# Optimization experiments

Hardware: AMD Instinct MI355X
Metric: run time of the kernel (lower is better)

Reference implementation:

```python
import jax, jax.numpy as jnp
import numpy as np
from jax.scipy.special import logsumexp

B, T, V, E, H, C, L = 128, 1024, 21, 32, 100, 20, 2


def setup_inputs() -> dict:
    key = jax.random.key(0)
    ks = jax.random.split(key, 32)
    def n(i, shape, scale=0.1):
        return (jax.random.normal(ks[i], shape) * scale).astype(jnp.float32)
    inp = {}
    inp["tokens"] = jax.random.randint(ks[0], (B, T), 0, V)
    inp["seq_lengths"] = jnp.full((B,), T, dtype=jnp.int32)
    inp["emb"] = n(1, (V, E), 1.0)
    idx = 2
    for l in range(L):
        din = E if l == 0 else 2 * H
        for sfx in ["", "_rev"]:
            inp[f"W_ih_l{l}{sfx}"] = n(idx, (4 * H, din)); idx += 1
            inp[f"W_hh_l{l}{sfx}"] = n(idx, (4 * H, H)); idx += 1
            inp[f"b_ih_l{l}{sfx}"] = n(idx, (4 * H,)); idx += 1
            inp[f"b_hh_l{l}{sfx}"] = n(idx, (4 * H,)); idx += 1
    inp["fW"] = n(idx, (C, 2 * H)); idx += 1
    inp["fb"] = n(idx, (C,)); idx += 1
    inp["gW"] = n(idx, (C * C, 2 * H)); idx += 1
    inp["gb"] = n(idx, (C * C,)); idx += 1
    inp["h0"] = n(idx, (2 * L, B, H), 1.0); idx += 1
    inp["c0"] = n(idx, (2 * L, B, H), 1.0)
    return inp


def _lstm_dir(x, Wih, Whh, bih, bhh, h0, c0, reverse):
    # x: [B,T,D]; precompute input projection once (PyTorch gate order i,f,g,o)
    xp = jnp.einsum('btd,gd->btg', x, Wih) + bih + bhh  # [B,T,4H]
    def step(carry, xt):
        h, c = carry
        gates = xt + h @ Whh.T
        i, f, g, o = jnp.split(gates, 4, axis=-1)
        c = jax.nn.sigmoid(f) * c + jax.nn.sigmoid(i) * jnp.tanh(g)
        h = jax.nn.sigmoid(o) * jnp.tanh(c)
        return (h, c), h
    _, hs = jax.lax.scan(step, (h0, c0), jnp.swapaxes(xp, 0, 1), reverse=reverse)
    return jnp.swapaxes(hs, 0, 1)  # [B,T,H]


def _crf_alpha(f, g):
    # alpha[0]=f[0]; alpha[t]=f[t]+LSE_i(alpha[t-1,i]+g[t,i,:])
    fs = jnp.swapaxes(f, 0, 1)  # [T,B,C]
    gs = jnp.swapaxes(g, 0, 1)  # [T,B,C,C]
    def step(a, fg):
        ft, gt = fg
        a = ft + logsumexp(a[:, :, None] + gt, axis=1)
        return a, a
    _, alphas = jax.lax.scan(step, fs[0], (fs[1:], gs[1:]))
    return jnp.swapaxes(jnp.concatenate([fs[:1], alphas], 0), 0, 1)


def _crf_beta(f, g):
    # beta[T-1]=0; beta[t]=LSE_j(g[t+1,:,j]+f[t+1,j]+beta[t+1,j])
    fs = jnp.swapaxes(f, 0, 1)
    gs = jnp.swapaxes(g, 0, 1)
    def step(b, fg):
        fnx, gnx = fg
        b = logsumexp(gnx + (fnx + b)[:, None, :], axis=2)
        return b, b
    bT = jnp.zeros_like(fs[0])
    _, betas = jax.lax.scan(step, bT, (fs[1:], gs[1:]), reverse=True)
    return jnp.swapaxes(jnp.concatenate([betas, bT[None]], 0), 0, 1)


def reference(tokens, seq_lengths, emb,
              W_ih_l0, W_hh_l0, b_ih_l0, b_hh_l0,
              W_ih_l0_rev, W_hh_l0_rev, b_ih_l0_rev, b_hh_l0_rev,
              W_ih_l1, W_hh_l1, b_ih_l1, b_hh_l1,
              W_ih_l1_rev, W_hh_l1_rev, b_ih_l1_rev, b_hh_l1_rev,
              fW, fb, gW, gb, h0, c0):
    x = emb[tokens]  # [B,T,E]
    # layer 0 (bidirectional)
    of = _lstm_dir(x, W_ih_l0, W_hh_l0, b_ih_l0, b_hh_l0, h0[0], c0[0], False)
    ob = _lstm_dir(x, W_ih_l0_rev, W_hh_l0_rev, b_ih_l0_rev, b_hh_l0_rev, h0[1], c0[1], True)
    x1 = jnp.concatenate([of, ob], axis=-1)  # dropout between layers: eval mode (identity)
    # layer 1
    of = _lstm_dir(x1, W_ih_l1, W_hh_l1, b_ih_l1, b_hh_l1, h0[2], c0[2], False)
    ob = _lstm_dir(x1, W_ih_l1_rev, W_hh_l1_rev, b_ih_l1_rev, b_hh_l1_rev, h0[3], c0[3], True)
    h = jnp.concatenate([of, ob], axis=-1)  # [B,T,2H]
    # pad_packed_sequence zeroes positions beyond seq_lengths
    mask = (jnp.arange(T)[None, :] < seq_lengths[:, None]).astype(h.dtype)
    h = h * mask[:, :, None]
    f_out = h @ fW.T + fb                      # [B,T,C] emissions
    g_out = (h @ gW.T + gb).reshape(B, T, C, C)  # [B,T,C,C] transitions
    alpha = _crf_alpha(f_out, g_out)
    beta = _crf_beta(f_out, g_out)
    logZ = logsumexp(alpha[:, -1], axis=-1)    # [B]
    log_marg = alpha + beta - logZ[:, None, None]
    return (jnp.exp(log_marg), f_out, g_out, alpha, beta)
```

## Files before the change

### kernel.cpp

```cpp
#include <hip/hip_runtime.h>
#include <hip/hip_bf16.h>

#define B_ 128
#define T_ 1024
#define E_ 32
#define H_ 100
#define C_ 20
#define M_ (B_*T_)

typedef __attribute__((ext_vector_type(8))) short bf16x8v;
typedef __attribute__((ext_vector_type(4))) float f32x4v;
typedef __attribute__((ext_vector_type(2))) _Float16 h2v;
typedef unsigned short u16;
typedef unsigned int u32;

static __device__ __forceinline__ short f2b(float x) {
  union { __hip_bfloat16 b; short s; } u;
  u.b = __float2bfloat16(x);
  return u.s;
}
static __device__ __forceinline__ float b2f(u16 x) {
  return __uint_as_float(((u32)x) << 16);
}

#if __has_builtin(__builtin_amdgcn_fdot2)
#define FDOT2(w, p, c) __builtin_amdgcn_fdot2((w), (p), (c), false)
#else
static __device__ __forceinline__ float FDOT2(h2v w, h2v p, float c) {
  return fmaf((float)w[1], (float)p[1], fmaf((float)w[0], (float)p[0], c));
}
#endif

#define WGBAR() do {                                        \
    asm volatile("s_waitcnt lgkmcnt(0)" ::: "memory");      \
    __builtin_amdgcn_s_barrier();                           \
    __builtin_amdgcn_sched_barrier(0);                      \
  } while (0)

__global__ void embed_k(const int* __restrict__ tok, const float* __restrict__ emb,
                        float* __restrict__ x0) {
  int idx = blockIdx.x * 256 + threadIdx.x;
  int bt = idx >> 5;
  int e  = idx & 31;
  x0[idx] = emb[tok[bt] * E_ + e];
}

template<int ABF, int OBF>
__global__ __launch_bounds__(256) void gemm_mfma_t(
    const void* __restrict__ Av, const float* __restrict__ W,
    const float* __restrict__ b1, const float* __restrict__ b2,
    void* __restrict__ Cv, int K, int N, int ldc)
{
  __shared__ short as[64 * 40];
  __shared__ short ws[64 * 40];
  const float* Af = (const float*)Av;
  const u16*   Ab = (const u16*)Av;
  float* Cf = (float*)Cv;
  u16*   Cb = (u16*)Cv;
  int tid = threadIdx.x, lane = tid & 63, w = tid >> 6;
  int lr = lane & 15, lq = lane >> 4;
  size_t m0 = (size_t)blockIdx.x * 64;
  int n0 = blockIdx.y * 64;
  int srow = tid >> 2;
  int sk = (tid & 3) * 8;
  bool wok = (n0 + srow) < N;
  const float* Wp = wok ? (W + (size_t)(n0 + srow) * K + sk) : W;
  size_t arow = (m0 + srow) * (size_t)K;
  f32x4v acc[4];
  #pragma unroll
  for (int r = 0; r < 4; ++r) acc[r] = (f32x4v){0.f, 0.f, 0.f, 0.f};
  int ksteps = (K + 31) / 32;
  for (int ks = 0; ks < ksteps; ++ks) {
    int kk = ks * 32;
    bf16x8v av, wv;
    if (kk + sk + 7 < K) {
      if (ABF) {
        av = *(const bf16x8v*)(Ab + arow + kk + sk);
      } else {
        float4 a0 = *(const float4*)(Af + arow + kk + sk);
        float4 a1 = *(const float4*)(Af + arow + kk + sk + 4);
        av[0]=f2b(a0.x); av[1]=f2b(a0.y); av[2]=f2b(a0.z); av[3]=f2b(a0.w);
        av[4]=f2b(a1.x); av[5]=f2b(a1.y); av[6]=f2b(a1.z); av[7]=f2b(a1.w);
      }
      if (wok) {
        float4 w0 = *(const float4*)(Wp + kk);
        float4 w1 = *(const float4*)(Wp + kk + 4);
        wv[0]=f2b(w0.x); wv[1]=f2b(w0.y); wv[2]=f2b(w0.z); wv[3]=f2b(w0.w);
        wv[4]=f2b(w1.x); wv[5]=f2b(w1.y); wv[6]=f2b(w1.z); wv[7]=f2b(w1.w);
      } else {
        #pragma unroll
        for (int j = 0; j < 8; ++j) wv[j] = 0;
      }
    } else {
      #pragma unroll
      for (int j = 0; j < 8; ++j) {
        int k = kk + sk + j;
        av[j] = (k < K) ? (ABF ? (short)Ab[arow + k] : f2b(Af[arow + k])) : (short)0;
        wv[j] = (wok && k < K) ? f2b(W[(size_t)(n0 + srow) * K + k]) : (short)0;
      }
    }
    *(bf16x8v*)&as[srow * 40 + sk] = av;
    *(bf16x8v*)&ws[srow * 40 + sk] = wv;
    __syncthreads();
    bf16x8v bf = *(const bf16x8v*)&ws[(16 * w + lr) * 40 + 8 * lq];
    #pragma unroll
    for (int r = 0; r < 4; ++r) {
      bf16x8v af = *(const bf16x8v*)&as[(16 * r + lr) * 40 + 8 * lq];
      acc[r] = __builtin_amdgcn_mfma_f32_16x16x32_bf16(af, bf, acc[r], 0, 0, 0);
    }
    __syncthreads();
  }
  int col = n0 + 16 * w + lr;
  if (col < N) {
    float bv = (b1 ? b1[col] : 0.f) + (b2 ? b2[col] : 0.f);
    #pragma unroll
    for (int r = 0; r < 4; ++r)
      #pragma unroll
      for (int rg = 0; rg < 4; ++rg) {
        size_t off = (m0 + 16 * r + 4 * lq + rg) * (size_t)ldc + col;
        float v = acc[r][rg] + bv;
        if (OBF) Cb[off] = (u16)f2b(v); else Cf[off] = v;
      }
  }
}

__global__ __launch_bounds__(512, 1) void lstm_scan(
    const u16* __restrict__ xp,
    const float* __restrict__ WhhF, const float* __restrict__ WhhR,
    const float* __restrict__ h0, const float* __restrict__ c0,
    const int* __restrict__ seqlen,
    u16* __restrict__ outbuf,
    int layer)
{
  int wg = blockIdx.x; int dir = wg & 1; int b = wg >> 1;
  int tid = threadIdx.x;
  const float* Whh = dir ? WhhR : WhhF;
  const u16* xpp = xp + ((size_t)dir * B_ + b) * T_ * 400;
  const float* h0p = h0 + ((size_t)(2 * layer + dir) * B_ + b) * H_;
  const float* c0p = c0 + ((size_t)(2 * layer + dir) * B_ + b) * H_;
  __shared__ __align__(16) float gsh[400];
  __shared__ __align__(16) _Float16 hph[112];
  bool act = (tid < 400);
  int r = tid >> 1, half = tid & 1;
  int bu = half * 24;
  u32 w0p[28], w1p[28];
  if (act) {
    const float* r0 = Whh + (size_t)(2 * r) * H_;
    const float* r1 = Whh + (size_t)(2 * r + 1) * H_;
    #pragma unroll
    for (int j = 0; j < 28; ++j) {
      int kp = bu + j;
      bool rl = half ? (j < 26) : (j < 24);
      int k = 2 * kp;
      float a0 = (rl && k < 100) ? r0[k] : 0.f;
      float a1 = (rl && k + 1 < 100) ? r0[k + 1] : 0.f;
      float b0 = (rl && k < 100) ? r1[k] : 0.f;
      float b1 = (rl && k + 1 < 100) ? r1[k + 1] : 0.f;
      w0p[j] = __builtin_bit_cast(u32, (h2v){(_Float16)a0, (_Float16)a1});
      w1p[j] = __builtin_bit_cast(u32, (h2v){(_Float16)b0, (_Float16)b1});
    }
    #pragma unroll
    for (int j = 0; j < 28; ++j)
      asm volatile("" : "+v"(w0p[j]), "+v"(w1p[j]));
  }
  if (tid < 112) hph[tid] = (_Float16)((tid < H_) ? h0p[tid] : 0.f);
  float c = (tid < H_) ? c0p[tid] : 0.f;
  int sl = seqlen ? seqlen[b] : T_;
  __syncthreads();
  int tstep = dir ? -1 : 1;
  int t0 = dir ? (T_ - 1) : 0;
  ushort2 xc = make_ushort2(0, 0), xn = make_ushort2(0, 0), x2 = make_ushort2(0, 0);
  bool ldx = act && !half;
  if (ldx) {
    xc = *(const ushort2*)(xpp + (size_t)t0 * 400 + 2 * r);
    xn = *(const ushort2*)(xpp + (size_t)(t0 + tstep) * 400 + 2 * r);
    x2 = *(const ushort2*)(xpp + (size_t)(t0 + 2 * tstep) * 400 + 2 * r);
  }
  for (int tt = 0; tt < T_; ++tt) {
    int t = t0 + tstep * tt;
    ushort2 x3 = make_ushort2(0, 0);
    if (ldx && tt + 3 < T_)
      x3 = *(const ushort2*)(xpp + (size_t)(t + 3 * tstep) * 400 + 2 * r);
    if (act) {
      float a0 = half ? 0.f : b2f(xc.x);
      float a1 = half ? 0.f : b2f(xc.y);
      #pragma unroll
      for (int q = 0; q < 7; ++q) {
        f32x4v hp = ((const f32x4v*)hph)[6 * half + q];
        #pragma unroll
        for (int i = 0; i < 4; ++i) {
          h2v p = __builtin_bit_cast(h2v, hp[i]);
          a0 = FDOT2(__builtin_bit_cast(h2v, w0p[4 * q + i]), p, a0);
          a1 = FDOT2(__builtin_bit_cast(h2v, w1p[4 * q + i]), p, a1);
        }
      }
      a0 += __shfl_xor(a0, 1);
      a1 += __shfl_xor(a1, 1);
      if (!half) *(float2*)&gsh[2 * r] = make_float2(a0, a1);
    }
    WGBAR();
    if (tid < H_) {
      float gi = gsh[tid], gf = gsh[H_ + tid], gg = gsh[2 * H_ + tid], go = gsh[3 * H_ + tid];
      float si = 1.f / (1.f + __expf(-gi));
      float sf = 1.f / (1.f + __expf(-gf));
      float so = 1.f / (1.f + __expf(-go));
      float tg = 1.f - 2.f / (1.f + __expf(2.f * gg));
      c = fmaf(sf, c, si * tg);
      float tc = 1.f - 2.f / (1.f + __expf(2.f * c));
      float h = so * tc;
      hph[tid] = (_Float16)h;
      outbuf[((size_t)b * T_ + t) * 200 + dir * H_ + tid] = (t < sl) ? (u16)f2b(h) : (u16)0;
    }
    WGBAR();
    xc = xn; xn = x2; x2 = x3;
  }
}

__global__ __launch_bounds__(64) void crf_k(
    const float* __restrict__ f, const float* __restrict__ g,
    float* __restrict__ alpha, float* __restrict__ beta)
{
  int wg = blockIdx.x;
  int lane = threadIdx.x;
  __shared__ __align__(16) float gl[4][400];
  __shared__ __align__(16) float aw[20];
  bool stv = lane < 50;
  int p0 = 8 * lane;
  float4 rA0, rA1, rB0, rB1;

  if (wg < B_) {
    int b = wg;
    const float* fp = f + (size_t)b * T_ * C_;
    const float* gp = g + (size_t)b * T_ * C_ * C_;
    float* ap = alpha + (size_t)b * T_ * C_;
    if (lane < C_) {
      float a0 = fp[lane];
      ap[lane] = a0;
      aw[lane] = a0;
    }
    if (stv) {
      float4 v0 = *(const float4*)(gp + 400 + p0);
      float4 v1 = *(const float4*)(gp + 404 + p0);
      *(float4*)&gl[1 & 3][p0] = v0;  *(float4*)&gl[1 & 3][p0 + 4] = v1;
      v0 = *(const float4*)(gp + 800 + p0);
      v1 = *(const float4*)(gp + 804 + p0);
      *(float4*)&gl[2 & 3][p0] = v0;  *(float4*)&gl[2 & 3][p0 + 4] = v1;
      rA0 = *(const float4*)(gp + 1200 + p0);
      rA1 = *(const float4*)(gp + 1204 + p0);
    }
    for (int t = 1; t < T_; ++t) {
      if (stv && (t + 3 < T_)) {
        rB0 = *(const float4*)(gp + (size_t)(t + 3) * 400 + p0);
        rB1 = *(const float4*)(gp + (size_t)(t + 3) * 400 + p0 + 4);
      }
      if (lane < C_) {
        const float* gr = &gl[t & 3][0];
        float ft = fp[(size_t)t * C_ + lane];
        float awv[20];
        #pragma unroll
        for (int q = 0; q < 5; ++q)
          *(f32x4v*)&awv[4 * q] = ((const f32x4v*)aw)[q];
        float s[20];
        #pragma unroll
        for (int i = 0; i < 20; ++i)
          s[i] = awv[i] + gr[i * 20 + lane];
        float m4[5];
        #pragma unroll
        for (int q = 0; q < 5; ++q)
          m4[q] = fmaxf(fmaxf(s[4*q], s[4*q+1]), fmaxf(s[4*q+2], s[4*q+3]));
        float m = fmaxf(fmaxf(m4[0], m4[1]), fmaxf(fmaxf(m4[2], m4[3]), m4[4]));
        float e4[5];
        #pragma unroll
        for (int q = 0; q < 5; ++q) {
          float e0 = __expf(s[4*q] - m),   e1 = __expf(s[4*q+1] - m);
          float e2 = __expf(s[4*q+2] - m), e3 = __expf(s[4*q+3] - m);
          e4[q] = (e0 + e1) + (e2 + e3);
        }
        float sum = (e4[0] + e4[1]) + ((e4[2] + e4[3]) + e4[4]);
        float an = ft + m + __logf(sum);
        ap[(size_t)t * C_ + lane] = an;
        aw[lane] = an;
      }
      if (stv && (t + 2 < T_)) {
        *(float4*)&gl[(t + 2) & 3][p0] = rA0;
        *(float4*)&gl[(t + 2) & 3][p0 + 4] = rA1;
      }
      rA0 = rB0; rA1 = rB1;
    }
  } else {
    int b = wg - B_;
    const float* fp = f + (size_t)b * T_ * C_;
    const float* gp = g + (size_t)b * T_ * C_ * C_;
    float* bp = beta + (size_t)b * T_ * C_;
    if (lane < C_) {
      bp[(size_t)(T_ - 1) * C_ + lane] = 0.f;
      aw[lane] = fp[(size_t)(T_ - 1) * C_ + lane];
    }
    if (stv) {
      float4 v0 = *(const float4*)(gp + (size_t)(T_ - 1) * 400 + p0);
      float4 v1 = *(const float4*)(gp + (size_t)(T_ - 1) * 400 + p0 + 4);
      *(float4*)&gl[(T_ - 1) & 3][p0] = v0;  *(float4*)&gl[(T_ - 1) & 3][p0 + 4] = v1;
      v0 = *(const float4*)(gp + (size_t)(T_ - 2) * 400 + p0);
      v1 = *(const float4*)(gp + (size_t)(T_ - 2) * 400 + p0 + 4);
      *(float4*)&gl[(T_ - 2) & 3][p0] = v0;  *(float4*)&gl[(T_ - 2) & 3][p0 + 4] = v1;
      rA0 = *(const float4*)(gp + (size_t)(T_ - 3) * 400 + p0);
      rA1 = *(const float4*)(gp + (size_t)(T_ - 3) * 400 + p0 + 4);
    }
    for (int u = 1; u < T_; ++u) {
      int t = T_ - 1 - u;
      int r = t + 1;
      if (stv && (r - 3 >= 1)) {
        rB0 = *(const float4*)(gp + (size_t)(r - 3) * 400 + p0);
        rB1 = *(const float4*)(gp + (size_t)(r - 3) * 400 + p0 + 4);
      }
      if (lane < C_) {
        const float* gr = &gl[r & 3][lane * 20];
        float fcur = fp[(size_t)t * C_ + lane];
        float awv[20];
        #pragma unroll
        for (int q = 0; q < 5; ++q)
          *(f32x4v*)&awv[4 * q] = ((const f32x4v*)aw)[q];
        float s[20];
        #pragma unroll
        for (int q = 0; q < 5; ++q) {
          f32x4v gq = *(const f32x4v*)&gr[4 * q];
          s[4*q]   = awv[4*q]   + gq[0];
          s[4*q+1] = awv[4*q+1] + gq[1];
          s[4*q+2] = awv[4*q+2] + gq[2];
          s[4*q+3] = awv[4*q+3] + gq[3];
        }
        float m4[5];
        #pragma unroll
        for (int q = 0; q < 5; ++q)
          m4[q] = fmaxf(fmaxf(s[4*q], s[4*q+1]), fmaxf(s[4*q+2], s[4*q+3]));
        float m = fmaxf(fmaxf(m4[0], m4[1]), fmaxf(fmaxf(m4[2], m4[3]), m4[4]));
        float e4[5];
        #pragma unroll
        for (int q = 0; q < 5; ++q) {
          float e0 = __expf(s[4*q] - m),   e1 = __expf(s[4*q+1] - m);
          float e2 = __expf(s[4*q+2] - m), e3 = __expf(s[4*q+3] - m);
          e4[q] = (e0 + e1) + (e2 + e3);
        }
        float sum = (e4[0] + e4[1]) + ((e4[2] + e4[3]) + e4[4]);
        float bn = m + __logf(sum);
        bp[(size_t)t * C_ + lane] = bn;
        aw[lane] = fcur + bn;
      }
      if (stv && (r - 2 >= 1)) {
        *(float4*)&gl[(r - 2) & 3][p0] = rA0;
        *(float4*)&gl[(r - 2) & 3][p0 + 4] = rA1;
      }
      rA0 = rB0; rA1 = rB1;
    }
  }
}

__global__ void logz_k(const float* __restrict__ alpha, float* __restrict__ lz) {
  int b = blockIdx.x; int lane = threadIdx.x;
  float a = (lane < C_) ? alpha[((size_t)b * T_ + (T_ - 1)) * C_ + lane] : -3.0e38f;
  float m = a;
  #pragma unroll
  for (int o = 32; o > 0; o >>= 1) m = fmaxf(m, __shfl_xor(m, o));
  float e = (lane < C_) ? __expf(a - m) : 0.f;
  #pragma unroll
  for (int o = 32; o > 0; o >>= 1) e += __shfl_xor(e, o);
  if (lane == 0) lz[b] = m + __logf(e);
}

__global__ void marg_k(const float* __restrict__ alpha, const float* __restrict__ beta,
                       const float* __restrict__ lz, float* __restrict__ out0) {
  size_t idx = (size_t)blockIdx.x * 256 + threadIdx.x;
  int b = (int)(idx / (T_ * C_));
  out0[idx] = __expf(alpha[idx] + beta[idx] - lz[b]);
}

extern "C" void kernel_launch(void* const* d_in, const int* in_sizes, int n_in,
                              void* d_out, int out_size, void* d_ws, size_t ws_size,
                              hipStream_t stream) {
  const int*   tok   = (const int*)d_in[0];
  const int*   seq   = (const int*)d_in[1];
  const float* emb   = (const float*)d_in[2];
  const float* Wih0  = (const float*)d_in[3];
  const float* Whh0  = (const float*)d_in[4];
  const float* bih0  = (const float*)d_in[5];
  const float* bhh0  = (const float*)d_in[6];
  const float* Wih0r = (const float*)d_in[7];
  const float* Whh0r = (const float*)d_in[8];
  const float* bih0r = (const float*)d_in[9];
  const float* bhh0r = (const float*)d_in[10];
  const float* Wih1  = (const float*)d_in[11];
  const float* Whh1  = (const float*)d_in[12];
  const float* bih1  = (const float*)d_in[13];
  const float* bhh1  = (const float*)d_in[14];
  const float* Wih1r = (const float*)d_in[15];
  const float* Whh1r = (const float*)d_in[16];
  const float* bih1r = (const float*)d_in[17];
  const float* bhh1r = (const float*)d_in[18];
  const float* fW    = (const float*)d_in[19];
  const float* fb    = (const float*)d_in[20];
  const float* gW    = (const float*)d_in[21];
  const float* gb    = (const float*)d_in[22];
  const float* h0    = (const float*)d_in[23];
  const float* c0    = (const float*)d_in[24];

  float* ws = (float*)d_ws;
  float* x0  = ws;
  u16*   xp  = (u16*)(ws + 4194304);
  u16*   x1  = (u16*)(ws + 109051904);
  float* lz  = ws + 135266304;

  float* out   = (float*)d_out;
  float* f_out = out + 2621440;
  float* g_out = out + 5242880;
  float* a_out = out + 57671680;
  float* b_out = out + 60293120;

  embed_k<<<16384, 256, 0, stream>>>(tok, emb, x0);

  dim3 g400(2048, 7), g20(2048, 1);
  gemm_mfma_t<0,1><<<g400, 256, 0, stream>>>(x0, Wih0,  bih0,  bhh0,  xp,                    32, 400, 400);
  gemm_mfma_t<0,1><<<g400, 256, 0, stream>>>(x0, Wih0r, bih0r, bhh0r, xp + (size_t)52428800, 32, 400, 400);
  lstm_scan<<<256, 512, 0, stream>>>(xp, Whh0, Whh0r, h0, c0, nullptr, x1, 0);
  gemm_mfma_t<1,1><<<g400, 256, 0, stream>>>(x1, Wih1,  bih1,  bhh1,  xp,                    200, 400, 400);
  gemm_mfma_t<1,1><<<g400, 256, 0, stream>>>(x1, Wih1r, bih1r, bhh1r, xp + (size_t)52428800, 200, 400, 400);
  lstm_scan<<<256, 512, 0, stream>>>(xp, Whh1, Whh1r, h0, c0, seq, x1, 1);
  gemm_mfma_t<1,0><<<g20,  256, 0, stream>>>(x1, fW, fb, nullptr, f_out, 200, 20,  20);
  gemm_mfma_t<1,0><<<g400, 256, 0, stream>>>(x1, gW, gb, nullptr, g_out, 200, 400, 400);
  crf_k<<<256, 64, 0, stream>>>(f_out, g_out, a_out, b_out);
  logz_k<<<128, 64, 0, stream>>>(a_out, lz);
  marg_k<<<10240, 256, 0, stream>>>(a_out, b_out, lz, out);
}
```

Baseline: 2.505 ms.

## Stage LSTM input projections in an LDS ring buffer with bulk prefetch

Replaces the per-step register prefetch of the input projection (three steps ahead from global memory) with a 128-step shared-memory ring buffer. Every 64 steps the whole workgroup does coalesced float4 loads of the next 64 steps into LDS, and each step reads its value from LDS. The goal is to take global-load latency off the serial recurrence critical path. In exchange the kernel uses about 100KB of LDS and has periodic bursts of load work inside the loop. There is no explicit barrier between writing the new chunk into the ring and reading it 64 steps later, so correctness depends on the per-step barriers.

```diff
diff --git a/kernel.cpp b/kernel.cpp
--- a/kernel.cpp
+++ b/kernel.cpp
@@ -138,6 +138,7 @@
   const u16* xpp = xp + ((size_t)dir * B_ + b) * T_ * 400;
   const float* h0p = h0 + ((size_t)(2 * layer + dir) * B_ + b) * H_;
   const float* c0p = c0 + ((size_t)(2 * layer + dir) * B_ + b) * H_;
+  __shared__ __align__(16) u16 xbuf[128 * 400];
   __shared__ __align__(16) float gsh[400];
   __shared__ __align__(16) _Float16 hph[112];
   bool act = (tid < 400);
@@ -166,24 +167,36 @@
   if (tid < 112) hph[tid] = (_Float16)((tid < H_) ? h0p[tid] : 0.f);
   float c = (tid < H_) ? c0p[tid] : 0.f;
   int sl = seqlen ? seqlen[b] : T_;
-  __syncthreads();
   int tstep = dir ? -1 : 1;
   int t0 = dir ? (T_ - 1) : 0;
-  ushort2 xc = make_ushort2(0, 0), xn = make_ushort2(0, 0), x2 = make_ushort2(0, 0);
-  bool ldx = act && !half;
-  if (ldx) {
-    xc = *(const ushort2*)(xpp + (size_t)t0 * 400 + 2 * r);
-    xn = *(const ushort2*)(xpp + (size_t)(t0 + tstep) * 400 + 2 * r);
-    x2 = *(const ushort2*)(xpp + (size_t)(t0 + 2 * tstep) * 400 + 2 * r);
-  }
+  #pragma unroll
+  for (int q = 0; q < 7; ++q) {
+    int idx = tid + q * 512;
+    if (idx < 3200) {
+      int si = idx / 50, r0i = (idx - 50 * si) * 8;
+      float4 v = *(const float4*)(xpp + (size_t)(t0 + tstep * si) * 400 + r0i);
+      *(float4*)&xbuf[si * 400 + r0i] = v;
+    }
+  }
+  __syncthreads();
   for (int tt = 0; tt < T_; ++tt) {
     int t = t0 + tstep * tt;
-    ushort2 x3 = make_ushort2(0, 0);
-    if (ldx && tt + 3 < T_)
-      x3 = *(const ushort2*)(xpp + (size_t)(t + 3 * tstep) * 400 + 2 * r);
+    if ((tt & 63) == 0 && tt + 64 < T_) {
+      #pragma unroll
+      for (int q = 0; q < 7; ++q) {
+        int idx = tid + q * 512;
+        if (idx < 3200) {
+          int si = idx / 50, r0i = (idx - 50 * si) * 8;
+          int ts = tt + 64 + si;
+          float4 v = *(const float4*)(xpp + (size_t)(t0 + tstep * ts) * 400 + r0i);
+          *(float4*)&xbuf[(ts & 127) * 400 + r0i] = v;
+        }
+      }
+    }
     if (act) {
-      float a0 = half ? 0.f : b2f(xc.x);
-      float a1 = half ? 0.f : b2f(xc.y);
+      ushort2 xc = make_ushort2(0, 0);
+      if (!half) xc = *(const ushort2*)&xbuf[(tt & 127) * 400 + 2 * r];
+      float a0 = 0.f, a1 = 0.f;
       #pragma unroll
       for (int q = 0; q < 7; ++q) {
         f32x4v hp = ((const f32x4v*)hph)[6 * half + q];
@@ -194,6 +207,7 @@
           a1 = FDOT2(__builtin_bit_cast(h2v, w1p[4 * q + i]), p, a1);
         }
       }
+      if (!half) { a0 += b2f(xc.x); a1 += b2f(xc.y); }
       a0 += __shfl_xor(a0, 1);
       a1 += __shfl_xor(a1, 1);
       if (!half) *(float2*)&gsh[2 * r] = make_float2(a0, a1);
@@ -212,7 +226,6 @@
       outbuf[((size_t)b * T_ + t) * 200 + dir * H_ + tid] = (t < sl) ? (u16)f2b(h) : (u16)0;
     }
     WGBAR();
-    xc = xn; xn = x2; x2 = x3;
   }
 }
 
```

After: 2.599 ms. 3.7% more time.
